# Kernel tuning notes

Hardware: AMD Instinct MI355X
Metric: run time of the kernel (lower is better)

Reference implementation:

```python
import jax, jax.numpy as jnp
import numpy as np

N = 50000      # num nodes
E = 1_600_000  # num edges
D = 64         # in_dim == hidden_dim
H = 4          # heads
C = 16         # head_dim = hidden_dim // heads
NEG = 0.2      # leaky_relu negative slope (PyG GATConv default)


def setup_inputs() -> dict:
    key = jax.random.key(0)
    ks = jax.random.split(key, 20)
    f = lambda k, s: (jax.random.normal(k, s, jnp.float32) * 0.1)
    return dict(
        node_features=jax.random.normal(ks[0], (N, D), jnp.float32),
        edge_index=jax.random.randint(ks[1], (2, E), 0, N, dtype=jnp.int32),
        edge_type=jax.random.randint(ks[2], (E,), 0, 5, dtype=jnp.int32),
        edge_attr=jax.random.normal(ks[3], (E, 1), jnp.float32),
        # GAT layer 1 (PyG GATConv: lin has no bias, att_* are [H,C], final bias [H*C])
        W1=f(ks[4], (D, H * C)), att_src1=f(ks[5], (H, C)), att_dst1=f(ks[6], (H, C)),
        We1=f(ks[7], (1, H * C)), att_e1=f(ks[8], (H, C)), b1=jnp.zeros((H * C,), jnp.float32),
        # GAT layer 2
        W2=f(ks[9], (D, H * C)), att_src2=f(ks[10], (H, C)), att_dst2=f(ks[11], (H, C)),
        We2=f(ks[12], (1, H * C)), att_e2=f(ks[13], (H, C)), b2=jnp.zeros((H * C,), jnp.float32),
        # LayerNorms
        g1=jnp.ones((D,), jnp.float32), beta1=jnp.zeros((D,), jnp.float32),
        g2=jnp.ones((D,), jnp.float32), beta2=jnp.zeros((D,), jnp.float32),
        # output head
        Wout=f(ks[14], (D, 1)), bout=jnp.zeros((1,), jnp.float32),
    )


def _layernorm(x, g, b, eps=1e-5):
    mu = x.mean(-1, keepdims=True)
    v = ((x - mu) ** 2).mean(-1, keepdims=True)
    return (x - mu) * jax.lax.rsqrt(v + eps) * g + b


def _seg_softmax(alpha, dst, n):
    # numerically stable segment softmax over incoming edges of each dst node
    m = jax.ops.segment_max(alpha, dst, num_segments=n)
    m = jnp.where(jnp.isfinite(m), m, 0.0)
    ex = jnp.exp(alpha - m[dst])
    den = jax.ops.segment_sum(ex, dst, num_segments=n)
    return ex / (den[dst] + 1e-16)


def _gatconv(x, src, dst, eattr, W, a_s, a_d, We, a_e, b, n):
    xs = (x @ W).reshape(n, H, C)                       # [N,H,C]
    a_src = jnp.einsum('nhc,hc->nh', xs, a_s)           # [N,H]
    a_dst = jnp.einsum('nhc,hc->nh', xs, a_d)           # [N,H]
    ee = (eattr @ We).reshape(-1, H, C)                 # [E',H,C]
    a_edge = jnp.einsum('ehc,hc->eh', ee, a_e)          # [E',H]
    alpha = a_src[src] + a_dst[dst] + a_edge            # [E',H]
    alpha = jax.nn.leaky_relu(alpha, NEG)
    alpha = _seg_softmax(alpha, dst, n)                 # [E',H]
    msg = xs[src] * alpha[..., None]                    # [E',H,C] gather-weighted messages
    out = jax.ops.segment_sum(msg, dst, num_segments=n) # scatter-aggregate
    return out.reshape(n, H * C) + b


def reference(node_features, edge_index, edge_type, edge_attr,
              W1, att_src1, att_dst1, We1, att_e1, b1,
              W2, att_src2, att_dst2, We2, att_e2, b2,
              g1, beta1, g2, beta2, Wout, bout):
    src, dst = edge_index[0], edge_index[1]
    # PyG add_self_loops(fill_value='mean'): self-loop edge_attr = mean of edge_attr over incoming edges
    cnt = jax.ops.segment_sum(jnp.ones((E,), jnp.float32), dst, num_segments=N)
    loop_attr = jax.ops.segment_sum(edge_attr, dst, num_segments=N) / jnp.maximum(cnt, 1.0)[:, None]
    loops = jnp.arange(N, dtype=src.dtype)
    src2 = jnp.concatenate([src, loops])
    dst2 = jnp.concatenate([dst, loops])
    ea = jnp.concatenate([edge_attr, loop_attr], axis=0)

    residual = node_features  # in_dim == hidden_dim -> no res_proj
    h = _gatconv(node_features, src2, dst2, ea, W1, att_src1, att_dst1, We1, att_e1, b1, N)
    h = jax.nn.elu(_layernorm(h + residual, g1, beta1))
    residual = h
    h = _gatconv(h, src2, dst2, ea, W2, att_src2, att_dst2, We2, att_e2, b2, N)
    h = jax.nn.elu(_layernorm(h + residual, g2, beta2))
    return h @ Wout + bout
```

## Files before the change

kernel.cpp:

```cpp
#include <hip/hip_runtime.h>
#include <hip/hip_bf16.h>
#include <cfloat>

#define NN 50000
#define NE 1600000
#define NEG 0.2f
#define NBKT 1563
#define BNODE 32
#define P1_TILE 2048
#define P1_BLOCKS 782
#define GEMM_BLOCKS 782
#define BCAP 1280
#define SLOTS 96
#define L2E 1.4426950408889634f
#define SMEM_BYTES 12512

typedef __attribute__((ext_vector_type(8))) short bf8_t;
typedef __attribute__((ext_vector_type(4))) float f4_t;

__device__ __forceinline__ float bf16bits_to_f(unsigned v) {
  return __uint_as_float(v << 16);
}
__device__ __forceinline__ unsigned f_to_bf16bits(float f) {
  unsigned u = __float_as_uint(f);
  return (u + 0x7fffu + ((u >> 16) & 1u)) >> 16;
}

__device__ __forceinline__ bf8_t pack8(const float* p) {
  bf8_t r;
#pragma unroll
  for (int i = 0; i < 8; ++i) r[i] = (short)f_to_bf16bits(p[i]);
  return r;
}

__device__ void bin_body(char* smem, int blk, const int* __restrict__ src,
                         const int* __restrict__ dst,
                         const float* __restrict__ ea, int* __restrict__ gcnt,
                         int2* __restrict__ gbuf) {
  int* lcnt = (int*)smem;
  int* lcur = lcnt + NBKT;
  int t = threadIdx.x;
  for (int i = t; i < NBKT; i += 256) lcnt[i] = 0;
  __syncthreads();
  int e0 = blk * P1_TILE;
  int bb[8], vx[8], vy[8];
#pragma unroll
  for (int k = 0; k < 8; ++k) {
    int e = e0 + k * 256 + t;
    if (e < NE) {
      int d = dst[e];
      bb[k] = d >> 5;
      vx[k] = ((d & 31) << 16) | src[e];
      vy[k] = __float_as_int(ea[e]);
      atomicAdd(&lcnt[bb[k]], 1);
    } else {
      bb[k] = -1;
    }
  }
  __syncthreads();
  for (int i = t; i < NBKT; i += 256) lcur[i] = atomicAdd(&gcnt[i], lcnt[i]);
  __syncthreads();
#pragma unroll
  for (int k = 0; k < 8; ++k) {
    if (bb[k] >= 0) {
      int pos = atomicAdd(&lcur[bb[k]], 1);
      if (pos < BCAP) gbuf[(size_t)bb[k] * BCAP + pos] = make_int2(vx[k], vy[k]);
    }
  }
}

template <bool FP32IN>
__device__ void gemm_body(char* smem, int blk, const void* __restrict__ xin,
                          const float* __restrict__ W,
                          const float* __restrict__ att_s,
                          const float* __restrict__ att_d,
                          unsigned short* __restrict__ xsb,
                          float* __restrict__ a_src,
                          float* __restrict__ a_dst) {
  unsigned short(*Wt)[68] = (unsigned short(*)[68])smem;
  int t = threadIdx.x;
  for (int i = t; i < 4096; i += 256) {
    int k = i >> 6, n = i & 63;
    Wt[n][k] = (unsigned short)f_to_bf16bits(W[i]);
  }
  __syncthreads();
  {
    int k = t & 63, h = t >> 6;
    float ps = 0.f, pd = 0.f;
#pragma unroll
    for (int c = 0; c < 16; ++c) {
      float w = bf16bits_to_f(Wt[h * 16 + c][k]);
      ps = fmaf(w, att_s[h * 16 + c], ps);
      pd = fmaf(w, att_d[h * 16 + c], pd);
    }
    Wt[64 + h][k] = (unsigned short)f_to_bf16bits(ps * L2E);
    Wt[68 + h][k] = (unsigned short)f_to_bf16bits(pd * L2E);
    Wt[72 + h][k] = 0;
    Wt[76 + h][k] = 0;
  }
  __syncthreads();
  int lane = t & 63, wave = t >> 6;
  int quad = lane >> 4, n16 = lane & 15;

  bf8_t bfrag[5][2];
#pragma unroll
  for (int nt = 0; nt < 5; ++nt)
#pragma unroll
    for (int kk = 0; kk < 2; ++kk)
      bfrag[nt][kk] = *(const bf8_t*)&Wt[nt * 16 + n16][kk * 32 + quad * 8];

  int r0 = blk * 64 + wave * 16;
  int rowA = r0 + n16; if (rowA > NN - 1) rowA = NN - 1;
  bf8_t af0, af1;
  if (FP32IN) {
    const float* xr = (const float*)xin + (size_t)rowA * 64 + quad * 8;
    af0 = pack8(xr);
    af1 = pack8(xr + 32);
  } else {
    const bf8_t* xrow =
        (const bf8_t*)((const unsigned short*)xin + (size_t)rowA * 64);
    af0 = xrow[quad];
    af1 = xrow[4 + quad];
  }
#pragma unroll
  for (int nt = 0; nt < 5; ++nt) {
    f4_t acc = {0.f, 0.f, 0.f, 0.f};
    acc = __builtin_amdgcn_mfma_f32_16x16x32_bf16(af0, bfrag[nt][0], acc, 0, 0, 0);
    acc = __builtin_amdgcn_mfma_f32_16x16x32_bf16(af1, bfrag[nt][1], acc, 0, 0, 0);
    if (nt < 4) {
#pragma unroll
      for (int reg = 0; reg < 4; ++reg) {
        int row = r0 + quad * 4 + reg;
        if (row < NN)
          xsb[(size_t)row * 64 + nt * 16 + n16] =
              (unsigned short)f_to_bf16bits(acc[reg]);
      }
    } else {
#pragma unroll
      for (int reg = 0; reg < 4; ++reg) {
        int row = r0 + quad * 4 + reg;
        if (row < NN && n16 < 8) {
          if (n16 < 4) a_src[row * 4 + n16] = acc[reg];
          else a_dst[row * 4 + (n16 - 4)] = acc[reg];
        }
      }
    }
  }
}

__global__ __launch_bounds__(256) void front_kernel(
    const int* __restrict__ src, const int* __restrict__ dst,
    const float* __restrict__ ea, int* __restrict__ gcnt,
    int2* __restrict__ gbuf, const float* __restrict__ x,
    const float* __restrict__ W1, const float* __restrict__ as1,
    const float* __restrict__ ad1, unsigned short* __restrict__ xsb,
    float* __restrict__ a_src, float* __restrict__ a_dst) {
  __shared__ __align__(16) char smem[SMEM_BYTES];
  if (blockIdx.x < P1_BLOCKS) {
    bin_body(smem, blockIdx.x, src, dst, ea, gcnt, gbuf);
  } else {
    gemm_body<true>(smem, blockIdx.x - P1_BLOCKS, x, W1, as1, ad1, xsb, a_src,
                    a_dst);
  }
}

__global__ __launch_bounds__(256) void gemm2_kernel(
    const unsigned short* __restrict__ xin, const float* __restrict__ W,
    const float* __restrict__ att_s, const float* __restrict__ att_d,
    unsigned short* __restrict__ xsb, float* __restrict__ a_src,
    float* __restrict__ a_dst) {
  __shared__ __align__(16) char smem[SMEM_BYTES];
  gemm_body<false>(smem, blockIdx.x, xin, W, att_s, att_d, xsb, a_src, a_dst);
}

__global__ __launch_bounds__(256) void build_kernel(
    const int* __restrict__ gcnt, const int2* __restrict__ gbuf,
    int* __restrict__ cnt, unsigned* __restrict__ csr) {
  __shared__ int lc[BNODE];
  int t = threadIdx.x;
  int b = blockIdx.x;
  if (t < BNODE) lc[t] = 0;
  __syncthreads();
  int len = gcnt[b]; if (len > BCAP) len = BCAP;
  const int2* buf = gbuf + (size_t)b * BCAP;
  for (int i = t; i < len; i += 256) {
    int2 v = buf[i];
    int dl = (v.x >> 16) & 31;
    int s = v.x & 0xffff;
    int pos = atomicAdd(&lc[dl], 1);
    if (pos < SLOTS) {
      unsigned eb = ((unsigned)v.y) & 0xffff0000u;
      csr[(size_t)(b * BNODE + dl) * SLOTS + pos] = eb | (unsigned)s;
    }
  }
  __syncthreads();
  if (t < BNODE) {
    int n = b * BNODE + t;
    if (n < NN) cnt[n] = min(lc[t], SLOTS);
  }
}

template <bool HEAD>
__global__ __launch_bounds__(256) void aggregate_kernel(
    const int* __restrict__ cnt, const unsigned* __restrict__ csr,
    const unsigned short* __restrict__ xsb, const float* __restrict__ a_src,
    const float* __restrict__ a_dst, const float* __restrict__ We,
    const float* __restrict__ att_e, const float* __restrict__ bias,
    const void* __restrict__ resv, const float* __restrict__ g,
    const float* __restrict__ beta, const float* __restrict__ Wout,
    const float* __restrict__ bout, float* __restrict__ out,
    unsigned short* __restrict__ out_b) {
  __shared__ __align__(16) uint2 rec[4][64][4];
  int t = threadIdx.x;
  int lane = t & 63, wave = t >> 6;
  int n = blockIdx.x * 4 + wave;
  int d2 = lane & 31;
  int hb = d2 >> 3;
  int half = lane >> 5;

  float sp = We[lane] * att_e[lane];
#pragma unroll
  for (int off = 8; off; off >>= 1) sp += __shfl_xor(sp, off, 16);
  sp *= L2E;
  float s0 = __shfl(sp, 0, 64), s1 = __shfl(sp, 16, 64);
  float s2 = __shfl(sp, 32, 64), s3 = __shfl(sp, 48, 64);

  const float4 adv = *(const float4*)(a_dst + (size_t)n * 4);

  int dn = cnt[n];
  int r0 = n * SLOTS, r1 = r0 + dn;
  float accx = 0.f, accy = 0.f, den = 0.f, easum = 0.f;
  const uint2* rpb = &rec[wave][half][hb];
  const char* xd = (const char*)xsb + d2 * 4;

  for (int base = r0; base < r1; base += 64) {
    int c = r1 - base; if (c > 64) c = 64;
    int e = base + lane;
    unsigned ce = (e < r1) ? csr[e] : 0u;
    float ea = __uint_as_float(ce & 0xffff0000u);
    easum += ea;
    unsigned soff = (ce & 0xffffu) * 128u;
    float ex0 = 0.f, ex1 = 0.f, ex2 = 0.f, ex3 = 0.f;
    if (e < r1) {
      const float4 av = *(const float4*)(a_src + (size_t)(ce & 0xffffu) * 4);
      float a0 = av.x + fmaf(ea, s0, adv.x); a0 = fmaxf(a0, NEG * a0);
      float a1 = av.y + fmaf(ea, s1, adv.y); a1 = fmaxf(a1, NEG * a1);
      float a2 = av.z + fmaf(ea, s2, adv.z); a2 = fmaxf(a2, NEG * a2);
      float a3 = av.w + fmaf(ea, s3, adv.w); a3 = fmaxf(a3, NEG * a3);
      ex0 = exp2f(a0); ex1 = exp2f(a1); ex2 = exp2f(a2); ex3 = exp2f(a3);
    }
    uint4* wp = (uint4*)&rec[wave][lane][0];
    wp[0] = make_uint4(soff, __float_as_uint(ex0), soff, __float_as_uint(ex1));
    wp[1] = make_uint4(soff, __float_as_uint(ex2), soff, __float_as_uint(ex3));
    int c8 = (c + 7) & ~7;
    for (int j = 0; j < c8; j += 8) {
      uint2 va = rpb[j * 4];
      uint2 vb = rpb[j * 4 + 8];
      uint2 vc = rpb[j * 4 + 16];
      uint2 vd = rpb[j * 4 + 24];
      unsigned ua = *(const unsigned*)(xd + va.x);
      unsigned ub = *(const unsigned*)(xd + vb.x);
      unsigned uc = *(const unsigned*)(xd + vc.x);
      unsigned ud = *(const unsigned*)(xd + vd.x);
      float efa = __uint_as_float(va.y), efb = __uint_as_float(vb.y);
      float efc = __uint_as_float(vc.y), efd = __uint_as_float(vd.y);
      den += (efa + efb) + (efc + efd);
      accx = fmaf(efa, __uint_as_float(ua << 16), accx);
      accy = fmaf(efa, __uint_as_float(ua & 0xffff0000u), accy);
      accx = fmaf(efb, __uint_as_float(ub << 16), accx);
      accy = fmaf(efb, __uint_as_float(ub & 0xffff0000u), accy);
      accx = fmaf(efc, __uint_as_float(uc << 16), accx);
      accy = fmaf(efc, __uint_as_float(uc & 0xffff0000u), accy);
      accx = fmaf(efd, __uint_as_float(ud << 16), accx);
      accy = fmaf(efd, __uint_as_float(ud & 0xffff0000u), accy);
    }
  }

  den += __shfl_xor(den, 32, 64);
  accx += __shfl_xor(accx, 32, 64);
  accy += __shfl_xor(accy, 32, 64);
#pragma unroll
  for (int off = 32; off; off >>= 1) easum += __shfl_xor(easum, off, 64);

  float loop_ea = easum / fmaxf((float)dn, 1.0f);
  float as_h = a_src[(size_t)n * 4 + hb];
  float adn = (hb == 0) ? adv.x : (hb == 1) ? adv.y : (hb == 2) ? adv.z : adv.w;
  float sph = (hb == 0) ? s0 : (hb == 1) ? s1 : (hb == 2) ? s2 : s3;
  float a_self = as_h + fmaf(loop_ea, sph, adn);
  a_self = fmaxf(a_self, NEG * a_self);
  float ex_self = exp2f(a_self);
  den += ex_self;
  unsigned un = *(const unsigned*)((const char*)xsb + (size_t)n * 128 + d2 * 4);
  accx = fmaf(ex_self, __uint_as_float(un << 16), accx);
  accy = fmaf(ex_self, __uint_as_float(un & 0xffff0000u), accy);

  float rden = 1.f / (den + 1e-16f);
  const float2 bi = *(const float2*)(bias + d2 * 2);
  float2 rsd;
  if (HEAD) {
    unsigned ur =
        *(const unsigned*)((const unsigned short*)resv + (size_t)n * 64 + d2 * 2);
    rsd.x = bf16bits_to_f(ur & 0xffffu);
    rsd.y = __uint_as_float(ur & 0xffff0000u);
  } else {
    rsd = *(const float2*)((const float*)resv + (size_t)n * 64 + d2 * 2);
  }
  float vx = accx * rden + bi.x + rsd.x;
  float vy = accy * rden + bi.y + rsd.y;
  float s = vx + vy;
#pragma unroll
  for (int off = 32; off; off >>= 1) s += __shfl_xor(s, off, 64);
  float mu = s * (1.0f / 128.0f);
  float dx = vx - mu, dy = vy - mu;
  float var = dx * dx + dy * dy;
#pragma unroll
  for (int off = 32; off; off >>= 1) var += __shfl_xor(var, off, 64);
  var *= (1.0f / 128.0f);
  float rstd = rsqrtf(var + 1e-5f);
  const float2 gg = *(const float2*)(g + d2 * 2);
  const float2 bb = *(const float2*)(beta + d2 * 2);
  float yx = dx * rstd * gg.x + bb.x;
  float yy = dy * rstd * gg.y + bb.y;
  yx = yx > 0.f ? yx : expm1f(yx);
  yy = yy > 0.f ? yy : expm1f(yy);
  if (HEAD) {
    const float2 wv = *(const float2*)(Wout + d2 * 2);
    float p = yx * wv.x + yy * wv.y;
#pragma unroll
    for (int off = 32; off; off >>= 1) p += __shfl_xor(p, off, 64);
    if (lane == 0) out[n] = p * 0.5f + bout[0];
  } else if (lane < 32) {
    unsigned ob = f_to_bf16bits(yx) | (f_to_bf16bits(yy) << 16);
    *(unsigned*)(out_b + (size_t)n * 64 + d2 * 2) = ob;
  }
}

extern "C" void kernel_launch(void* const* d_in, const int* in_sizes, int n_in,
                              void* d_out, int out_size, void* d_ws,
                              size_t ws_size, hipStream_t stream) {
  const float* node_features = (const float*)d_in[0];
  const int* edge_index = (const int*)d_in[1];
  const int* src = edge_index;
  const int* dst = edge_index + NE;
  const float* edge_attr = (const float*)d_in[3];
  const float* W1 = (const float*)d_in[4];
  const float* att_src1 = (const float*)d_in[5];
  const float* att_dst1 = (const float*)d_in[6];
  const float* We1 = (const float*)d_in[7];
  const float* att_e1 = (const float*)d_in[8];
  const float* b1 = (const float*)d_in[9];
  const float* W2 = (const float*)d_in[10];
  const float* att_src2 = (const float*)d_in[11];
  const float* att_dst2 = (const float*)d_in[12];
  const float* We2 = (const float*)d_in[13];
  const float* att_e2 = (const float*)d_in[14];
  const float* b2 = (const float*)d_in[15];
  const float* g1 = (const float*)d_in[16];
  const float* beta1 = (const float*)d_in[17];
  const float* g2 = (const float*)d_in[18];
  const float* beta2 = (const float*)d_in[19];
  const float* Wout = (const float*)d_in[20];
  const float* bout = (const float*)d_in[21];
  float* out = (float*)d_out;

  char* ws = (char*)d_ws;
  size_t o = 0;
  auto alloc = [&](size_t bytes) {
    void* p = ws + o;
    o += (bytes + 255) & ~(size_t)255;
    return p;
  };
  int* gcnt = (int*)alloc((size_t)NBKT * 4);
  int2* gbuf = (int2*)alloc((size_t)NBKT * BCAP * 8);
  int* cnt = (int*)alloc((size_t)NN * 4);
  unsigned* csr = (unsigned*)alloc((size_t)NN * SLOTS * 4);
  unsigned short* xsb = (unsigned short*)alloc((size_t)NN * 64 * 2);
  unsigned short* h1b = (unsigned short*)alloc((size_t)NN * 64 * 2);
  float* a_srcb = (float*)alloc((size_t)NN * 4 * 4);
  float* a_dstb = (float*)alloc((size_t)NN * 4 * 4);

  hipMemsetAsync(gcnt, 0, (size_t)NBKT * 4, stream);

  front_kernel<<<P1_BLOCKS + GEMM_BLOCKS, 256, 0, stream>>>(
      src, dst, edge_attr, gcnt, gbuf, node_features, W1, att_src1, att_dst1,
      xsb, a_srcb, a_dstb);
  build_kernel<<<NBKT, 256, 0, stream>>>(gcnt, gbuf, cnt, csr);

  aggregate_kernel<false><<<NN / 4, 256, 0, stream>>>(
      cnt, csr, xsb, a_srcb, a_dstb, We1, att_e1, b1, node_features, g1, beta1,
      nullptr, nullptr, nullptr, h1b);

  gemm2_kernel<<<GEMM_BLOCKS, 256, 0, stream>>>(h1b, W2, att_src2, att_dst2,
                                                xsb, a_srcb, a_dstb);
  aggregate_kernel<true><<<NN / 4, 256, 0, stream>>>(
      cnt, csr, xsb, a_srcb, a_dstb, We2, att_e2, b2, h1b, g2, beta2, Wout,
      bout, out, nullptr);
}
```

Before: 254.5 us.

## Build CSR directly with global atomics, removing the bucket pass and build kernel

The two-stage binning (shared-memory bucket counts into a global bucket buffer, then a separate build kernel that scatters into per-node CSR slots) is replaced by direct per-edge global atomicAdd on per-node counters and an immediate write into the CSR slot. Edge loads are vectorized as int4. This removes one kernel launch and the intermediate gbuf round-trip. In exchange it issues 1.6M contended global atomics with scattered writes, and the aggregate kernel now clamps the count to SLOTS.

Measured after the change: 361.1 us. 41.9% more time.

```diff
diff --git a/kernel.cpp b/kernel.cpp
--- a/kernel.cpp
+++ b/kernel.cpp
@@ -5,15 +5,12 @@
 #define NN 50000
 #define NE 1600000
 #define NEG 0.2f
-#define NBKT 1563
-#define BNODE 32
 #define P1_TILE 2048
 #define P1_BLOCKS 782
 #define GEMM_BLOCKS 782
-#define BCAP 1280
 #define SLOTS 96
 #define L2E 1.4426950408889634f
-#define SMEM_BYTES 12512
+#define SMEM_BYTES 10880
 
 typedef __attribute__((ext_vector_type(8))) short bf8_t;
 typedef __attribute__((ext_vector_type(4))) float f4_t;
@@ -33,38 +30,38 @@
   return r;
 }
 
-__device__ void bin_body(char* smem, int blk, const int* __restrict__ src,
+__device__ void bin_body(int blk, const int* __restrict__ src,
                          const int* __restrict__ dst,
-                         const float* __restrict__ ea, int* __restrict__ gcnt,
-                         int2* __restrict__ gbuf) {
-  int* lcnt = (int*)smem;
-  int* lcur = lcnt + NBKT;
+                         const float* __restrict__ ea, int* __restrict__ cnt,
+                         unsigned* __restrict__ csr) {
   int t = threadIdx.x;
-  for (int i = t; i < NBKT; i += 256) lcnt[i] = 0;
-  __syncthreads();
-  int e0 = blk * P1_TILE;
-  int bb[8], vx[8], vy[8];
-#pragma unroll
-  for (int k = 0; k < 8; ++k) {
-    int e = e0 + k * 256 + t;
-    if (e < NE) {
-      int d = dst[e];
-      bb[k] = d >> 5;
-      vx[k] = ((d & 31) << 16) | src[e];
-      vy[k] = __float_as_int(ea[e]);
-      atomicAdd(&lcnt[bb[k]], 1);
-    } else {
-      bb[k] = -1;
-    }
-  }
-  __syncthreads();
-  for (int i = t; i < NBKT; i += 256) lcur[i] = atomicAdd(&gcnt[i], lcnt[i]);
-  __syncthreads();
-#pragma unroll
-  for (int k = 0; k < 8; ++k) {
-    if (bb[k] >= 0) {
-      int pos = atomicAdd(&lcur[bb[k]], 1);
-      if (pos < BCAP) gbuf[(size_t)bb[k] * BCAP + pos] = make_int2(vx[k], vy[k]);
+  int e0 = blk * P1_TILE + t * 8;
+  if (e0 + 8 <= NE) {
+    int4 d0 = *(const int4*)(dst + e0), d1 = *(const int4*)(dst + e0 + 4);
+    int4 s0 = *(const int4*)(src + e0), s1 = *(const int4*)(src + e0 + 4);
+    int4 a0 = *(const int4*)((const int*)ea + e0);
+    int4 a1 = *(const int4*)((const int*)ea + e0 + 4);
+    int dd[8] = {d0.x, d0.y, d0.z, d0.w, d1.x, d1.y, d1.z, d1.w};
+    int ss[8] = {s0.x, s0.y, s0.z, s0.w, s1.x, s1.y, s1.z, s1.w};
+    int aa[8] = {a0.x, a0.y, a0.z, a0.w, a1.x, a1.y, a1.z, a1.w};
+#pragma unroll
+    for (int k = 0; k < 8; ++k) {
+      int pos = atomicAdd(&cnt[dd[k]], 1);
+      if (pos < SLOTS)
+        csr[(size_t)dd[k] * SLOTS + pos] =
+            (((unsigned)aa[k]) & 0xffff0000u) | (unsigned)ss[k];
+    }
+  } else {
+    for (int k = 0; k < 8; ++k) {
+      int e = e0 + k;
+      if (e < NE) {
+        int d = dst[e];
+        int pos = atomicAdd(&cnt[d], 1);
+        if (pos < SLOTS)
+          csr[(size_t)d * SLOTS + pos] =
+              (((unsigned)__float_as_uint(ea[e])) & 0xffff0000u) |
+              (unsigned)src[e];
+      }
     }
   }
 }
@@ -150,14 +147,14 @@
 
 __global__ __launch_bounds__(256) void front_kernel(
     const int* __restrict__ src, const int* __restrict__ dst,
-    const float* __restrict__ ea, int* __restrict__ gcnt,
-    int2* __restrict__ gbuf, const float* __restrict__ x,
+    const float* __restrict__ ea, int* __restrict__ cnt,
+    unsigned* __restrict__ csr, const float* __restrict__ x,
     const float* __restrict__ W1, const float* __restrict__ as1,
     const float* __restrict__ ad1, unsigned short* __restrict__ xsb,
     float* __restrict__ a_src, float* __restrict__ a_dst) {
   __shared__ __align__(16) char smem[SMEM_BYTES];
   if (blockIdx.x < P1_BLOCKS) {
-    bin_body(smem, blockIdx.x, src, dst, ea, gcnt, gbuf);
+    bin_body(blockIdx.x, src, dst, ea, cnt, csr);
   } else {
     gemm_body<true>(smem, blockIdx.x - P1_BLOCKS, x, W1, as1, ad1, xsb, a_src,
                     a_dst);
@@ -171,33 +168,6 @@
     float* __restrict__ a_dst) {
   __shared__ __align__(16) char smem[SMEM_BYTES];
   gemm_body<false>(smem, blockIdx.x, xin, W, att_s, att_d, xsb, a_src, a_dst);
-}
-
-__global__ __launch_bounds__(256) void build_kernel(
-    const int* __restrict__ gcnt, const int2* __restrict__ gbuf,
-    int* __restrict__ cnt, unsigned* __restrict__ csr) {
-  __shared__ int lc[BNODE];
-  int t = threadIdx.x;
-  int b = blockIdx.x;
-  if (t < BNODE) lc[t] = 0;
-  __syncthreads();
-  int len = gcnt[b]; if (len > BCAP) len = BCAP;
-  const int2* buf = gbuf + (size_t)b * BCAP;
-  for (int i = t; i < len; i += 256) {
-    int2 v = buf[i];
-    int dl = (v.x >> 16) & 31;
-    int s = v.x & 0xffff;
-    int pos = atomicAdd(&lc[dl], 1);
-    if (pos < SLOTS) {
-      unsigned eb = ((unsigned)v.y) & 0xffff0000u;
-      csr[(size_t)(b * BNODE + dl) * SLOTS + pos] = eb | (unsigned)s;
-    }
-  }
-  __syncthreads();
-  if (t < BNODE) {
-    int n = b * BNODE + t;
-    if (n < NN) cnt[n] = min(lc[t], SLOTS);
-  }
 }
 
 template <bool HEAD>
@@ -227,7 +197,7 @@
 
   const float4 adv = *(const float4*)(a_dst + (size_t)n * 4);
 
-  int dn = cnt[n];
+  int dn = cnt[n]; if (dn > SLOTS) dn = SLOTS;
   int r0 = n * SLOTS, r1 = r0 + dn;
   float accx = 0.f, accy = 0.f, den = 0.f, easum = 0.f;
   const uint2* rpb = &rec[wave][half][hb];
@@ -370,8 +340,6 @@
     o += (bytes + 255) & ~(size_t)255;
     return p;
   };
-  int* gcnt = (int*)alloc((size_t)NBKT * 4);
-  int2* gbuf = (int2*)alloc((size_t)NBKT * BCAP * 8);
   int* cnt = (int*)alloc((size_t)NN * 4);
   unsigned* csr = (unsigned*)alloc((size_t)NN * SLOTS * 4);
   unsigned short* xsb = (unsigned short*)alloc((size_t)NN * 64 * 2);
@@ -379,12 +347,11 @@
   float* a_srcb = (float*)alloc((size_t)NN * 4 * 4);
   float* a_dstb = (float*)alloc((size_t)NN * 4 * 4);
 
-  hipMemsetAsync(gcnt, 0, (size_t)NBKT * 4, stream);
+  hipMemsetAsync(cnt, 0, (size_t)NN * 4, stream);
 
   front_kernel<<<P1_BLOCKS + GEMM_BLOCKS, 256, 0, stream>>>(
-      src, dst, edge_attr, gcnt, gbuf, node_features, W1, att_src1, att_dst1,
+      src, dst, edge_attr, cnt, csr, node_features, W1, att_src1, att_dst1,
       xsb, a_srcb, a_dstb);
-  build_kernel<<<NBKT, 256, 0, stream>>>(gcnt, gbuf, cnt, csr);
 
   aggregate_kernel<false><<<NN / 4, 256, 0, stream>>>(
       cnt, csr, xsb, a_srcb, a_dstb, We1, att_e1, b1, node_features, g1, beta1,
```

## Fuse CSR build into aggregation kernels using per-block shared-memory buckets

Applied to the files above, without the earlier changes.

Removes the separate build_kernel and its global CSR/cnt arrays. Each aggregation block now reads its destination bucket from gbuf, scatters edges into a shared-memory per-node slot table, then 8 waves each aggregate 4 nodes from shared memory. This saves a launch and the global CSR write/read traffic. In exchange the bucket-sorting work runs twice (once per layer), blocks are larger, and each wave processes nodes serially, which may hurt load balance and occupancy.

Result: slower. 278.3 us (+9.3%).

```diff
diff --git a/kernel.cpp b/kernel.cpp
--- a/kernel.cpp
+++ b/kernel.cpp
@@ -173,75 +173,34 @@
   gemm_body<false>(smem, blockIdx.x, xin, W, att_s, att_d, xsb, a_src, a_dst);
 }
 
-__global__ __launch_bounds__(256) void build_kernel(
-    const int* __restrict__ gcnt, const int2* __restrict__ gbuf,
-    int* __restrict__ cnt, unsigned* __restrict__ csr) {
-  __shared__ int lc[BNODE];
-  int t = threadIdx.x;
-  int b = blockIdx.x;
-  if (t < BNODE) lc[t] = 0;
-  __syncthreads();
-  int len = gcnt[b]; if (len > BCAP) len = BCAP;
-  const int2* buf = gbuf + (size_t)b * BCAP;
-  for (int i = t; i < len; i += 256) {
-    int2 v = buf[i];
-    int dl = (v.x >> 16) & 31;
-    int s = v.x & 0xffff;
-    int pos = atomicAdd(&lc[dl], 1);
-    if (pos < SLOTS) {
-      unsigned eb = ((unsigned)v.y) & 0xffff0000u;
-      csr[(size_t)(b * BNODE + dl) * SLOTS + pos] = eb | (unsigned)s;
-    }
-  }
-  __syncthreads();
-  if (t < BNODE) {
-    int n = b * BNODE + t;
-    if (n < NN) cnt[n] = min(lc[t], SLOTS);
-  }
-}
-
 template <bool HEAD>
-__global__ __launch_bounds__(256) void aggregate_kernel(
-    const int* __restrict__ cnt, const unsigned* __restrict__ csr,
+__device__ __forceinline__ void agg_node(
+    int n, int lane, const unsigned* crow, int dn, uint2* recw,
     const unsigned short* __restrict__ xsb, const float* __restrict__ a_src,
-    const float* __restrict__ a_dst, const float* __restrict__ We,
-    const float* __restrict__ att_e, const float* __restrict__ bias,
-    const void* __restrict__ resv, const float* __restrict__ g,
-    const float* __restrict__ beta, const float* __restrict__ Wout,
-    const float* __restrict__ bout, float* __restrict__ out,
-    unsigned short* __restrict__ out_b) {
-  __shared__ __align__(16) uint2 rec[4][64][4];
-  int t = threadIdx.x;
-  int lane = t & 63, wave = t >> 6;
-  int n = blockIdx.x * 4 + wave;
+    const float* __restrict__ a_dst, float s0, float s1, float s2, float s3,
+    const float* __restrict__ bias, const void* __restrict__ resv,
+    const float* __restrict__ g, const float* __restrict__ beta,
+    const float* __restrict__ Wout, const float* __restrict__ bout,
+    float* __restrict__ out, unsigned short* __restrict__ out_b) {
   int d2 = lane & 31;
   int hb = d2 >> 3;
   int half = lane >> 5;
 
-  float sp = We[lane] * att_e[lane];
-#pragma unroll
-  for (int off = 8; off; off >>= 1) sp += __shfl_xor(sp, off, 16);
-  sp *= L2E;
-  float s0 = __shfl(sp, 0, 64), s1 = __shfl(sp, 16, 64);
-  float s2 = __shfl(sp, 32, 64), s3 = __shfl(sp, 48, 64);
-
   const float4 adv = *(const float4*)(a_dst + (size_t)n * 4);
 
-  int dn = cnt[n];
-  int r0 = n * SLOTS, r1 = r0 + dn;
   float accx = 0.f, accy = 0.f, den = 0.f, easum = 0.f;
-  const uint2* rpb = &rec[wave][half][hb];
+  const uint2* rpb = recw + half * 4 + hb;
   const char* xd = (const char*)xsb + d2 * 4;
 
-  for (int base = r0; base < r1; base += 64) {
-    int c = r1 - base; if (c > 64) c = 64;
-    int e = base + lane;
-    unsigned ce = (e < r1) ? csr[e] : 0u;
+  for (int base = 0; base < dn; base += 64) {
+    int c = dn - base; if (c > 64) c = 64;
+    int i = base + lane;
+    unsigned ce = (i < dn) ? crow[i] : 0u;
     float ea = __uint_as_float(ce & 0xffff0000u);
     easum += ea;
     unsigned soff = (ce & 0xffffu) * 128u;
     float ex0 = 0.f, ex1 = 0.f, ex2 = 0.f, ex3 = 0.f;
-    if (e < r1) {
+    if (i < dn) {
       const float4 av = *(const float4*)(a_src + (size_t)(ce & 0xffffu) * 4);
       float a0 = av.x + fmaf(ea, s0, adv.x); a0 = fmaxf(a0, NEG * a0);
       float a1 = av.y + fmaf(ea, s1, adv.y); a1 = fmaxf(a1, NEG * a1);
@@ -249,7 +208,7 @@
       float a3 = av.w + fmaf(ea, s3, adv.w); a3 = fmaxf(a3, NEG * a3);
       ex0 = exp2f(a0); ex1 = exp2f(a1); ex2 = exp2f(a2); ex3 = exp2f(a3);
     }
-    uint4* wp = (uint4*)&rec[wave][lane][0];
+    uint4* wp = (uint4*)(recw + (size_t)lane * 4);
     wp[0] = make_uint4(soff, __float_as_uint(ex0), soff, __float_as_uint(ex1));
     wp[1] = make_uint4(soff, __float_as_uint(ex2), soff, __float_as_uint(ex3));
     int c8 = (c + 7) & ~7;
@@ -332,6 +291,55 @@
   } else if (lane < 32) {
     unsigned ob = f_to_bf16bits(yx) | (f_to_bf16bits(yy) << 16);
     *(unsigned*)(out_b + (size_t)n * 64 + d2 * 2) = ob;
+  }
+}
+
+template <bool HEAD>
+__global__ __launch_bounds__(512) void agg_kernel(
+    const int* __restrict__ gcnt, const int2* __restrict__ gbuf,
+    const unsigned short* __restrict__ xsb, const float* __restrict__ a_src,
+    const float* __restrict__ a_dst, const float* __restrict__ We,
+    const float* __restrict__ att_e, const float* __restrict__ bias,
+    const void* __restrict__ resv, const float* __restrict__ g,
+    const float* __restrict__ beta, const float* __restrict__ Wout,
+    const float* __restrict__ bout, float* __restrict__ out,
+    unsigned short* __restrict__ out_b) {
+  __shared__ int lc[BNODE];
+  __shared__ __align__(16) unsigned csr_l[BNODE][SLOTS];
+  __shared__ __align__(16) uint2 rec[8][64][4];
+  int t = threadIdx.x;
+  int b = blockIdx.x;
+  if (t < BNODE) lc[t] = 0;
+  __syncthreads();
+  int len = gcnt[b]; if (len > BCAP) len = BCAP;
+  const int2* buf = gbuf + (size_t)b * BCAP;
+  for (int i = t; i < len; i += 512) {
+    int2 v = buf[i];
+    int dl = (v.x >> 16) & 31;
+    int pos = atomicAdd(&lc[dl], 1);
+    if (pos < SLOTS)
+      csr_l[dl][pos] =
+          (((unsigned)v.y) & 0xffff0000u) | (unsigned)(v.x & 0xffff);
+  }
+  __syncthreads();
+
+  int lane = t & 63, wave = t >> 6;
+  float sp = We[lane] * att_e[lane];
+#pragma unroll
+  for (int off = 8; off; off >>= 1) sp += __shfl_xor(sp, off, 16);
+  sp *= L2E;
+  float s0 = __shfl(sp, 0, 64), s1 = __shfl(sp, 16, 64);
+  float s2 = __shfl(sp, 32, 64), s3 = __shfl(sp, 48, 64);
+  uint2* recw = &rec[wave][0][0];
+
+#pragma unroll 1
+  for (int k = 0; k < 4; ++k) {
+    int dl = wave * 4 + k;
+    int n = b * BNODE + dl;
+    if (n >= NN) break;
+    int dn = lc[dl]; if (dn > SLOTS) dn = SLOTS;
+    agg_node<HEAD>(n, lane, &csr_l[dl][0], dn, recw, xsb, a_src, a_dst, s0, s1,
+                   s2, s3, bias, resv, g, beta, Wout, bout, out, out_b);
   }
 }
 
@@ -372,8 +380,6 @@
   };
   int* gcnt = (int*)alloc((size_t)NBKT * 4);
   int2* gbuf = (int2*)alloc((size_t)NBKT * BCAP * 8);
-  int* cnt = (int*)alloc((size_t)NN * 4);
-  unsigned* csr = (unsigned*)alloc((size_t)NN * SLOTS * 4);
   unsigned short* xsb = (unsigned short*)alloc((size_t)NN * 64 * 2);
   unsigned short* h1b = (unsigned short*)alloc((size_t)NN * 64 * 2);
   float* a_srcb = (float*)alloc((size_t)NN * 4 * 4);
@@ -384,15 +390,14 @@
   front_kernel<<<P1_BLOCKS + GEMM_BLOCKS, 256, 0, stream>>>(
       src, dst, edge_attr, gcnt, gbuf, node_features, W1, att_src1, att_dst1,
       xsb, a_srcb, a_dstb);
-  build_kernel<<<NBKT, 256, 0, stream>>>(gcnt, gbuf, cnt, csr);
-
-  aggregate_kernel<false><<<NN / 4, 256, 0, stream>>>(
-      cnt, csr, xsb, a_srcb, a_dstb, We1, att_e1, b1, node_features, g1, beta1,
-      nullptr, nullptr, nullptr, h1b);
+
+  agg_kernel<false><<<NBKT, 512, 0, stream>>>(
+      gcnt, gbuf, xsb, a_srcb, a_dstb, We1, att_e1, b1, node_features, g1,
+      beta1, nullptr, nullptr, nullptr, h1b);
 
   gemm2_kernel<<<GEMM_BLOCKS, 256, 0, stream>>>(h1b, W2, att_src2, att_dst2,
                                                 xsb, a_srcb, a_dstb);
-  aggregate_kernel<true><<<NN / 4, 256, 0, stream>>>(
-      cnt, csr, xsb, a_srcb, a_dstb, We2, att_e2, b2, h1b, g2, beta2, Wout,
+  agg_kernel<true><<<NBKT, 512, 0, stream>>>(
+      gcnt, gbuf, xsb, a_srcb, a_dstb, We2, att_e2, b2, h1b, g2, beta2, Wout,
       bout, out, nullptr);
 }
```

## Fuse layer-2 projection GEMM into layer-1 aggregation epilogue

Applied to the files above, without the earlier changes.

Removes the separate gemm2 kernel and instead computes each node's layer-2 projection and attention logits inside the layer-1 aggregate kernel. Each wave multiplies its fresh LayerNorm/ELU output by a bf16-packed W2 held in shared memory, using shuffles and scalar FMAs. The results go into a reused region of the binning buffer, so the ping-pong avoids clobbering xsb. This saves a launch and a full reload of h1. The cost is every block converting W2 (8 KB of extra LDS, possibly lower occupancy) and scalar FMAs replacing MFMA.

Measured after the change: 285.3 us. 1.12x slower.

```diff
diff --git a/kernel.cpp b/kernel.cpp
--- a/kernel.cpp
+++ b/kernel.cpp
@@ -69,8 +69,7 @@
   }
 }
 
-template <bool FP32IN>
-__device__ void gemm_body(char* smem, int blk, const void* __restrict__ xin,
+__device__ void gemm_body(char* smem, int blk, const float* __restrict__ xin,
                           const float* __restrict__ W,
                           const float* __restrict__ att_s,
                           const float* __restrict__ att_d,
@@ -111,17 +110,9 @@
 
   int r0 = blk * 64 + wave * 16;
   int rowA = r0 + n16; if (rowA > NN - 1) rowA = NN - 1;
-  bf8_t af0, af1;
-  if (FP32IN) {
-    const float* xr = (const float*)xin + (size_t)rowA * 64 + quad * 8;
-    af0 = pack8(xr);
-    af1 = pack8(xr + 32);
-  } else {
-    const bf8_t* xrow =
-        (const bf8_t*)((const unsigned short*)xin + (size_t)rowA * 64);
-    af0 = xrow[quad];
-    af1 = xrow[4 + quad];
-  }
+  const float* xr = xin + (size_t)rowA * 64 + quad * 8;
+  bf8_t af0 = pack8(xr);
+  bf8_t af1 = pack8(xr + 32);
 #pragma unroll
   for (int nt = 0; nt < 5; ++nt) {
     f4_t acc = {0.f, 0.f, 0.f, 0.f};
@@ -159,18 +150,9 @@
   if (blockIdx.x < P1_BLOCKS) {
     bin_body(smem, blockIdx.x, src, dst, ea, gcnt, gbuf);
   } else {
-    gemm_body<true>(smem, blockIdx.x - P1_BLOCKS, x, W1, as1, ad1, xsb, a_src,
-                    a_dst);
-  }
-}
-
-__global__ __launch_bounds__(256) void gemm2_kernel(
-    const unsigned short* __restrict__ xin, const float* __restrict__ W,
-    const float* __restrict__ att_s, const float* __restrict__ att_d,
-    unsigned short* __restrict__ xsb, float* __restrict__ a_src,
-    float* __restrict__ a_dst) {
-  __shared__ __align__(16) char smem[SMEM_BYTES];
-  gemm_body<false>(smem, blockIdx.x, xin, W, att_s, att_d, xsb, a_src, a_dst);
+    gemm_body(smem, blockIdx.x - P1_BLOCKS, x, W1, as1, ad1, xsb, a_src,
+              a_dst);
+  }
 }
 
 __global__ __launch_bounds__(256) void build_kernel(
@@ -209,9 +191,22 @@
     const void* __restrict__ resv, const float* __restrict__ g,
     const float* __restrict__ beta, const float* __restrict__ Wout,
     const float* __restrict__ bout, float* __restrict__ out,
-    unsigned short* __restrict__ out_b) {
+    unsigned short* __restrict__ out_b, const float* __restrict__ W2,
+    const float* __restrict__ as2v, const float* __restrict__ ad2v,
+    unsigned short* __restrict__ xsb2, float* __restrict__ a_src2,
+    float* __restrict__ a_dst2) {
   __shared__ __align__(16) uint2 rec[4][64][4];
+  __shared__ unsigned W2p[32][64];
   int t = threadIdx.x;
+  if (!HEAD) {
+    for (int i = t; i < 2048; i += 256) {
+      int m = i >> 6, j = i & 63;
+      unsigned lo = f_to_bf16bits(W2[(2 * m) * 64 + j]);
+      unsigned hi = f_to_bf16bits(W2[(2 * m + 1) * 64 + j]);
+      W2p[m][j] = lo | (hi << 16);
+    }
+    __syncthreads();
+  }
   int lane = t & 63, wave = t >> 6;
   int n = blockIdx.x * 4 + wave;
   int d2 = lane & 31;
@@ -329,9 +324,36 @@
 #pragma unroll
     for (int off = 32; off; off >>= 1) p += __shfl_xor(p, off, 64);
     if (lane == 0) out[n] = p * 0.5f + bout[0];
-  } else if (lane < 32) {
+    return;
+  }
+  if (lane < 32) {
     unsigned ob = f_to_bf16bits(yx) | (f_to_bf16bits(yy) << 16);
     *(unsigned*)(out_b + (size_t)n * 64 + d2 * 2) = ob;
+  }
+
+  {
+    int j = lane;
+    float acc2 = 0.f;
+    const unsigned* wcol = &W2p[0][j];
+#pragma unroll 8
+    for (int m = 0; m < 32; ++m) {
+      unsigned w = wcol[m * 64];
+      float h0 = __shfl(yx, m, 32);
+      float h1v = __shfl(yy, m, 32);
+      acc2 = fmaf(h0, __uint_as_float(w << 16), acc2);
+      acc2 = fmaf(h1v, __uint_as_float(w & 0xffff0000u), acc2);
+    }
+    xsb2[(size_t)n * 64 + j] = (unsigned short)f_to_bf16bits(acc2);
+    float ps = acc2 * as2v[j], pd = acc2 * ad2v[j];
+#pragma unroll
+    for (int off = 8; off; off >>= 1) {
+      ps += __shfl_xor(ps, off, 16);
+      pd += __shfl_xor(pd, off, 16);
+    }
+    if ((lane & 15) == 0) {
+      a_src2[(size_t)n * 4 + (j >> 4)] = ps * L2E;
+      a_dst2[(size_t)n * 4 + (j >> 4)] = pd * L2E;
+    }
   }
 }
 
@@ -378,6 +400,9 @@
   unsigned short* h1b = (unsigned short*)alloc((size_t)NN * 64 * 2);
   float* a_srcb = (float*)alloc((size_t)NN * 4 * 4);
   float* a_dstb = (float*)alloc((size_t)NN * 4 * 4);
+  unsigned short* xsb2 = (unsigned short*)gbuf;
+  float* a_src2 = (float*)((char*)gbuf + 6400000);
+  float* a_dst2 = (float*)((char*)gbuf + 7200000);
 
   hipMemsetAsync(gcnt, 0, (size_t)NBKT * 4, stream);
 
@@ -388,11 +413,11 @@
 
   aggregate_kernel<false><<<NN / 4, 256, 0, stream>>>(
       cnt, csr, xsb, a_srcb, a_dstb, We1, att_e1, b1, node_features, g1, beta1,
-      nullptr, nullptr, nullptr, h1b);
-
-  gemm2_kernel<<<GEMM_BLOCKS, 256, 0, stream>>>(h1b, W2, att_src2, att_dst2,
-                                                xsb, a_srcb, a_dstb);
+      nullptr, nullptr, nullptr, h1b, W2, att_src2, att_dst2, xsb2, a_src2,
+      a_dst2);
+
   aggregate_kernel<true><<<NN / 4, 256, 0, stream>>>(
-      cnt, csr, xsb, a_srcb, a_dstb, We2, att_e2, b2, h1b, g2, beta2, Wout,
-      bout, out, nullptr);
-}
+      cnt, csr, xsb2, a_src2, a_dst2, We2, att_e2, b2, h1b, g2, beta2, Wout,
+      bout, out, nullptr, nullptr, nullptr, nullptr, nullptr, nullptr,
+      nullptr);
+}
```
